# Kernel tuning notes

Measured on AMD Instinct MI355X. Metric: run time of the kernel, lower is better.

The kernel has to match this reference:

```python
import jax, jax.numpy as jnp
import numpy as np

B, S, D, H = 4, 1024, 1024, 16
DK = D // H
NEG = -1e9


def setup_inputs() -> dict:
    key = jax.random.key(0)
    ks = jax.random.split(key, 14)
    sc = 1.0 / np.sqrt(D)
    inp = {
        "query": jax.random.normal(ks[0], (B, S, D), jnp.float32),
        "key": jax.random.normal(ks[1], (B, S, D), jnp.float32),
        "value": jax.random.normal(ks[2], (B, S, D), jnp.float32),
        "mask": jax.random.randint(ks[3], (B, S, S), 0, 2, jnp.int32),
        "group_prob": jax.random.uniform(ks[4], (B, S, S), jnp.float32),
        "Wq": jax.random.normal(ks[5], (D, D), jnp.float32) * sc,
        "bq": jnp.zeros((D,), jnp.float32),
        "Wk": jax.random.normal(ks[6], (D, D), jnp.float32) * sc,
        "bk": jnp.zeros((D,), jnp.float32),
        "Wv": jax.random.normal(ks[7], (D, D), jnp.float32) * sc,
        "bv": jnp.zeros((D,), jnp.float32),
        "Wo": jax.random.normal(ks[8], (D, D), jnp.float32) * sc,
        "bo": jnp.zeros((D,), jnp.float32),
    }
    return inp


def reference(query, key, value, mask, group_prob, Wq, bq, Wk, bk, Wv, bv, Wo, bo):
    # QKV projections, split heads: [B,S,D] -> [B,H,S,DK]
    def proj(x, W, b):
        return (x @ W.T + b).reshape(B, S, H, DK).transpose(0, 2, 1, 3)

    q = proj(query, Wq, bq)
    k = proj(key, Wk, bk)
    v = proj(value, Wv, bv)

    scores = jnp.einsum("bhqd,bhkd->bhqk", q, k) / jnp.sqrt(jnp.float32(DK))

    # group_prob branch: allowed where mask OR diagonal is nonzero
    diag = jnp.eye(S, dtype=jnp.int32)
    allowed = (mask[:, None, :, :] | diag[None, None, :, :]) != 0  # [B,1,S,S]
    scores = jnp.where(allowed, scores, NEG)

    p_attn = jax.nn.softmax(scores, axis=-1)
    p_attn = p_attn * group_prob[:, None, :, :]  # post-softmax group reweighting

    x = jnp.einsum("bhqk,bhkd->bhqd", p_attn, v)
    x = x.transpose(0, 2, 1, 3).reshape(B, S, D)
    return x @ Wo.T + bo
```

## Files before the change

kernel.cpp:

```cpp
#include <hip/hip_runtime.h>
#include <hip/hip_bf16.h>


#define AS1q __attribute__((address_space(1)))
#define AS3q __attribute__((address_space(3)))

typedef __attribute__((ext_vector_type(8))) __bf16 bf16x8;
typedef __attribute__((ext_vector_type(4))) float f32x4;
typedef __attribute__((ext_vector_type(8))) unsigned short u16x8;

#define GSTR 40

__device__ __forceinline__ void gload_lds16(const void* g, void* l) {
  __builtin_amdgcn_global_load_lds((const AS1q void*)g, (AS3q void*)l, 16, 0, 0);
}
__device__ __forceinline__ bf16x8 lds_read8(const unsigned short* p) {
  bf16x8 r;
  __builtin_memcpy(&r, __builtin_assume_aligned(p, 16), 16);
  return r;
}
__device__ __forceinline__ void lds_write8(unsigned short* p, const void* v) {
  __builtin_memcpy(__builtin_assume_aligned(p, 16), v, 16);
}
__device__ __forceinline__ u16x8 cvt8h(const float4 a, const float4 b) {
  const float fv[8] = {a.x, a.y, a.z, a.w, b.x, b.y, b.z, b.w};
  union { u16x8 v; __bf16 e[8]; } hh;
#pragma unroll
  for (int i = 0; i < 8; ++i) hh.e[i] = (__bf16)fv[i];
  return hh.v;
}
__device__ __forceinline__ void cvt8hl(const float4 a, const float4 b, u16x8* hi, u16x8* lo) {
  const float fv[8] = {a.x, a.y, a.z, a.w, b.x, b.y, b.z, b.w};
  union { u16x8 v; __bf16 e[8]; } hh, ll;
#pragma unroll
  for (int i = 0; i < 8; ++i) {
    const __bf16 h = (__bf16)fv[i];
    hh.e[i] = h;
    ll.e[i] = (__bf16)(fv[i] - (float)h);
  }
  *hi = hh.v; *lo = ll.v;
}
__device__ __forceinline__ unsigned short bfbits(float f) {
  const __bf16 h = (__bf16)f;
  unsigned short u; __builtin_memcpy(&u, &h, 2); return u;
}

__global__ __launch_bounds__(256) void k_gemm_qkv(
    const float* __restrict__ X0, const float* __restrict__ X1, const float* __restrict__ X2,
    const float* __restrict__ W0, const float* __restrict__ W1, const float* __restrict__ W2,
    const float* __restrict__ B0, const float* __restrict__ B1, const float* __restrict__ B2,
    unsigned short* __restrict__ O0, unsigned short* __restrict__ O1,
    unsigned short* __restrict__ O2)
{
  const int z = blockIdx.z;
  const float* X = (z == 0) ? X0 : (z == 1) ? X1 : X2;
  const float* W = (z == 0) ? W0 : (z == 1) ? W1 : W2;
  const float* Bi = (z == 0) ? B0 : (z == 1) ? B1 : B2;
  unsigned short* O = (z == 0) ? O0 : (z == 1) ? O1 : O2;

  const int bid = blockIdx.x;
  const int swz = (bid & 7) * 64 + (bid >> 3);
  const int n0 = (swz & 15) * 64, m0 = (swz >> 4) * 128;

  __shared__ alignas(16) unsigned short Ah[128 * GSTR];
  __shared__ alignas(16) unsigned short Bh[64 * GSTR];
  const int tid = threadIdx.x, l = tid & 63, w = tid >> 6;
  const int wr = w >> 1, wc = w & 1;

  f32x4 acc[4][2];
#pragma unroll
  for (int i = 0; i < 4; ++i)
#pragma unroll
    for (int j = 0; j < 2; ++j) acc[i][j] = (f32x4){0.f, 0.f, 0.f, 0.f};

  const int arow = tid >> 1, ac0 = (tid & 1) * 16;
  const int brow = tid >> 2, bc0 = (tid & 3) * 8;
  const float* xsrc = X + (size_t)(m0 + arow) * 1024 + ac0;
  const float* wsrc = W + (size_t)(n0 + brow) * 1024 + bc0;

  float4 fx[4], fw[2];
#pragma unroll
  for (int i = 0; i < 4; ++i) fx[i] = *(const float4*)(xsrc + i * 4);
#pragma unroll
  for (int i = 0; i < 2; ++i) fw[i] = *(const float4*)(wsrc + i * 4);

  for (int kt = 0; kt < 32; ++kt) {
    u16x8 xh[2], wh1;
    xh[0] = cvt8h(fx[0], fx[1]);
    xh[1] = cvt8h(fx[2], fx[3]);
    wh1 = cvt8h(fw[0], fw[1]);
    if (kt < 31) {
      const float* nx = xsrc + (kt + 1) * 32;
      const float* nw = wsrc + (kt + 1) * 32;
#pragma unroll
      for (int i = 0; i < 4; ++i) fx[i] = *(const float4*)(nx + i * 4);
#pragma unroll
      for (int i = 0; i < 2; ++i) fw[i] = *(const float4*)(nw + i * 4);
    }
    __syncthreads();
    lds_write8(&Ah[arow * GSTR + ac0], &xh[0]);
    lds_write8(&Ah[arow * GSTR + ac0 + 8], &xh[1]);
    lds_write8(&Bh[brow * GSTR + bc0], &wh1);
    __syncthreads();

    bf16x8 ah[4], bh[2];
#pragma unroll
    for (int mf = 0; mf < 4; ++mf) {
      const int r = wr * 64 + mf * 16 + (l & 15);
      ah[mf] = lds_read8(&Ah[r * GSTR + (l >> 4) * 8]);
    }
#pragma unroll
    for (int nf = 0; nf < 2; ++nf) {
      const int r = wc * 32 + nf * 16 + (l & 15);
      bh[nf] = lds_read8(&Bh[r * GSTR + (l >> 4) * 8]);
    }
#pragma unroll
    for (int mf = 0; mf < 4; ++mf)
#pragma unroll
      for (int nf = 0; nf < 2; ++nf)
        acc[mf][nf] = __builtin_amdgcn_mfma_f32_16x16x32_bf16(ah[mf], bh[nf], acc[mf][nf], 0, 0, 0);
  }

#pragma unroll
  for (int nf = 0; nf < 2; ++nf) {
    const int col = n0 + wc * 32 + nf * 16 + (l & 15);
    const float bias = Bi[col];
#pragma unroll
    for (int mf = 0; mf < 4; ++mf) {
      const int rbase = m0 + wr * 64 + mf * 16 + (l >> 4) * 4;
#pragma unroll
      for (int j = 0; j < 4; ++j)
        O[(size_t)(rbase + j) * 1024 + col] = bfbits(acc[mf][nf][j] + bias);
    }
  }
}

__global__ __launch_bounds__(256) void k_gemm_out(
    const unsigned short* __restrict__ X, const float* __restrict__ W,
    const float* __restrict__ Bi, float* __restrict__ Out)
{
  const int bid = blockIdx.x;
  const int swz = (bid & 7) * 128 + (bid >> 3);
  const int n0 = (swz & 15) * 64, m0 = (swz >> 4) * 64;

  __shared__ alignas(16) unsigned short Ah[64 * GSTR];
  __shared__ alignas(16) unsigned short Bh[64 * GSTR], Bl[64 * GSTR];
  const int tid = threadIdx.x, l = tid & 63, w = tid >> 6;
  const int wr = w >> 1, wc = w & 1;

  f32x4 acc[2][2];
#pragma unroll
  for (int i = 0; i < 2; ++i)
#pragma unroll
    for (int j = 0; j < 2; ++j) acc[i][j] = (f32x4){0.f, 0.f, 0.f, 0.f};

  const int srow = tid >> 2, sc0 = (tid & 3) * 8;
  const unsigned short* xsrc = X + (size_t)(m0 + srow) * 1024 + sc0;
  const float* wsrc = W + (size_t)(n0 + srow) * 1024 + sc0;

  u16x8 xcur = *(const u16x8*)xsrc;
  float4 fw[2];
#pragma unroll
  for (int i = 0; i < 2; ++i) fw[i] = *(const float4*)(wsrc + i * 4);

  for (int kt = 0; kt < 32; ++kt) {
    const u16x8 xstage = xcur;
    u16x8 wh1, wl1;
    cvt8hl(fw[0], fw[1], &wh1, &wl1);
    if (kt < 31) {
      xcur = *(const u16x8*)(xsrc + (kt + 1) * 32);
      const float* nw = wsrc + (kt + 1) * 32;
#pragma unroll
      for (int i = 0; i < 2; ++i) fw[i] = *(const float4*)(nw + i * 4);
    }
    __syncthreads();
    lds_write8(&Ah[srow * GSTR + sc0], &xstage);
    lds_write8(&Bh[srow * GSTR + sc0], &wh1);
    lds_write8(&Bl[srow * GSTR + sc0], &wl1);
    __syncthreads();

    bf16x8 ah[2], bh[2], bl[2];
#pragma unroll
    for (int mf = 0; mf < 2; ++mf) {
      const int r = wr * 32 + mf * 16 + (l & 15);
      ah[mf] = lds_read8(&Ah[r * GSTR + (l >> 4) * 8]);
    }
#pragma unroll
    for (int nf = 0; nf < 2; ++nf) {
      const int r = wc * 32 + nf * 16 + (l & 15);
      bh[nf] = lds_read8(&Bh[r * GSTR + (l >> 4) * 8]);
      bl[nf] = lds_read8(&Bl[r * GSTR + (l >> 4) * 8]);
    }
#pragma unroll
    for (int mf = 0; mf < 2; ++mf)
#pragma unroll
      for (int nf = 0; nf < 2; ++nf) {
        acc[mf][nf] = __builtin_amdgcn_mfma_f32_16x16x32_bf16(ah[mf], bh[nf], acc[mf][nf], 0, 0, 0);
        acc[mf][nf] = __builtin_amdgcn_mfma_f32_16x16x32_bf16(ah[mf], bl[nf], acc[mf][nf], 0, 0, 0);
      }
  }

#pragma unroll
  for (int nf = 0; nf < 2; ++nf) {
    const int col = n0 + wc * 32 + nf * 16 + (l & 15);
    const float bias = Bi[col];
#pragma unroll
    for (int mf = 0; mf < 2; ++mf) {
      const int rbase = m0 + wr * 32 + mf * 16 + (l >> 4) * 4;
#pragma unroll
      for (int j = 0; j < 4; ++j)
        Out[(size_t)(rbase + j) * 1024 + col] = acc[mf][nf][j] + bias;
    }
  }
}

__global__ __launch_bounds__(256) void k_attn(
    const unsigned short* Qh, const unsigned short* __restrict__ Kb,
    const unsigned short* __restrict__ Vb,
    const int* __restrict__ Mask, const float* __restrict__ Gp,
    unsigned short* Xo)
{
  const int i = blockIdx.x;
  const int xc = i & 7, kk_ = i >> 3;
  const int h = kk_ & 15, g = kk_ >> 4;
  const int qb = g * 8 + xc;
  const int qt = qb >> 2, b = qb & 3;

  __shared__ alignas(16) unsigned short Kh[2][64 * 64];
  __shared__ alignas(16) unsigned short Vh[64 * 64];
  __shared__ alignas(16) unsigned short Ph[64 * 64];
  __shared__ alignas(16) int Ms[64 * 64];
  __shared__ alignas(16) float Gs[64 * 64];
  const int tid = threadIdx.x, l = tid & 63, w = tid >> 6;

  const unsigned short* kb_ = Kb + (size_t)b * 1048576 + h * 64;
  const unsigned short* vb_ = Vb + (size_t)b * 1048576 + h * 64;
  const int qrowbase = b * 1024 + qt * 64;

  bf16x8 aq[2];
  {
    const int qrow = qt * 64 + w * 16 + (l & 15);
    const unsigned short* qp_ = Qh + ((size_t)(b * 1024 + qrow)) * 1024 + h * 64;
    aq[0] = lds_read8(qp_ + (l >> 4) * 8);
    aq[1] = lds_read8(qp_ + 32 + (l >> 4) * 8);
  }

  f32x4 accO[4];
#pragma unroll
  for (int nf = 0; nf < 4; ++nf) accO[nf] = (f32x4){0.f, 0.f, 0.f, 0.f};
  float zacc[4] = {0.f, 0.f, 0.f, 0.f};

  const int qloc0 = w * 16 + (l >> 4) * 4;
  const int qg0 = qt * 64 + qloc0;
  const int mcol = l & 15;

  const int srcg8 = ((l & 7) ^ (l >> 3)) * 8;
  const int rowl = l >> 3;

  const int* msrc = Mask + ((size_t)(qrowbase + w * 16 + (l >> 4)) << 10) + (l & 15) * 4;
  const float* gsrc = Gp + ((size_t)(qrowbase + w * 16 + (l >> 4)) << 10) + (l & 15) * 4;

  const int kb4 = (tid & 15) * 4, db4 = (tid >> 4) * 4;
  union U4 { unsigned int u[2]; unsigned short s[4]; };
  U4 vr[4];

#pragma unroll
  for (int I = 0; I < 2; ++I)
    gload_lds16(kb_ + (size_t)(I * 32 + w * 8 + rowl) * 1024 + srcg8,
                &Kh[0][I * 2048 + w * 512]);
#pragma unroll
  for (int ii = 0; ii < 4; ++ii)
    __builtin_memcpy(&vr[ii], vb_ + (size_t)(kb4 + ii) * 1024 + db4, 8);

  int buf = 0;
  for (int kt = 0; kt < 16; ++kt) {
    __syncthreads();

#pragma unroll
    for (int I = 0; I < 4; ++I) {
      gload_lds16(msrc + (size_t)kt * 64 + I * 4096, (char*)Ms + w * 4096 + I * 1024);
      gload_lds16(gsrc + (size_t)kt * 64 + I * 4096, (char*)Gs + w * 4096 + I * 1024);
    }
#pragma unroll
    for (int ii = 0; ii < 4; ++ii) {
      const int d = db4 + ii;
      union { unsigned short s[4]; unsigned long long v; } pk;
#pragma unroll
      for (int u = 0; u < 4; ++u) pk.s[u] = vr[u].s[ii];
      const int c = kb4 ^ ((d & 7) << 3);
      __builtin_memcpy(__builtin_assume_aligned(&Vh[d * 64 + c], 8), &pk.v, 8);
    }
    __syncthreads();

    if (kt < 15) {
#pragma unroll
      for (int I = 0; I < 2; ++I)
        gload_lds16(kb_ + (size_t)((kt + 1) * 64 + I * 32 + w * 8 + rowl) * 1024 + srcg8,
                    &Kh[buf ^ 1][I * 2048 + w * 512]);
#pragma unroll
      for (int ii = 0; ii < 4; ++ii)
        __builtin_memcpy(&vr[ii], vb_ + (size_t)((kt + 1) * 64 + kb4 + ii) * 1024 + db4, 8);
    }

#pragma unroll
    for (int nf = 0; nf < 4; ++nf) {
      f32x4 sacc = (f32x4){0.f, 0.f, 0.f, 0.f};
      const int kr = nf * 16 + (l & 15);
#pragma unroll
      for (int ks = 0; ks < 2; ++ks) {
        const int c = (ks * 32 + (l >> 4) * 8) ^ ((kr & 7) << 3);
        sacc = __builtin_amdgcn_mfma_f32_16x16x32_bf16(aq[ks], lds_read8(&Kh[buf][kr * 64 + c]), sacc, 0, 0, 0);
      }
      const int kg = kt * 64 + nf * 16 + mcol;
#pragma unroll
      for (int j = 0; j < 4; ++j) {
        const int qg = qg0 + j;
        const int qloc = qloc0 + j;
        const int mk = Ms[qloc * 64 + nf * 16 + mcol];
        const float gvv = Gs[qloc * 64 + nf * 16 + mcol];
        const int allowed = mk | (qg == kg);
        const float e = allowed ? exp2f(fmaf(sacc[j], 0.18033688f, -17.31234049f)) : 0.f;
        zacc[j] += e;
        Ph[qloc * 64 + ((nf * 16 + mcol) ^ ((qloc & 7) << 3))] = bfbits(e * gvv);
      }
    }
    bf16x8 pah[2];
    {
      const int ar = w * 16 + (l & 15);
#pragma unroll
      for (int ks = 0; ks < 2; ++ks) {
        const int c = (ks * 32 + (l >> 4) * 8) ^ ((ar & 7) << 3);
        pah[ks] = lds_read8(&Ph[ar * 64 + c]);
      }
    }
#pragma unroll
    for (int nf = 0; nf < 4; ++nf) {
      const int dr = nf * 16 + (l & 15);
#pragma unroll
      for (int ks = 0; ks < 2; ++ks) {
        const int c = (ks * 32 + (l >> 4) * 8) ^ ((dr & 7) << 3);
        accO[nf] = __builtin_amdgcn_mfma_f32_16x16x32_bf16(pah[ks], lds_read8(&Vh[dr * 64 + c]), accO[nf], 0, 0, 0);
      }
    }
    buf ^= 1;
  }

#pragma unroll
  for (int j = 0; j < 4; ++j) {
#pragma unroll
    for (int off = 1; off < 16; off <<= 1) zacc[j] += __shfl_xor(zacc[j], off, 64);
  }
  float rz[4];
#pragma unroll
  for (int j = 0; j < 4; ++j) rz[j] = 1.f / zacc[j];

#pragma unroll
  for (int nf = 0; nf < 4; ++nf) {
    const int d = nf * 16 + (l & 15);
#pragma unroll
    for (int j = 0; j < 4; ++j) {
      const int qg = qg0 + j;
      Xo[((size_t)(b * 1024 + qg)) * 1024 + h * 64 + d] = bfbits(accO[nf][j] * rz[j]);
    }
  }
}

extern "C" void kernel_launch(void* const* d_in, const int* in_sizes, int n_in,
                              void* d_out, int out_size, void* d_ws, size_t ws_size,
                              hipStream_t stream) {
  const float* query = (const float*)d_in[0];
  const float* key_in = (const float*)d_in[1];
  const float* value = (const float*)d_in[2];
  const int* mask = (const int*)d_in[3];
  const float* gp = (const float*)d_in[4];
  const float* Wq = (const float*)d_in[5];
  const float* bq = (const float*)d_in[6];
  const float* Wk = (const float*)d_in[7];
  const float* bk = (const float*)d_in[8];
  const float* Wv = (const float*)d_in[9];
  const float* bv = (const float*)d_in[10];
  const float* Wo = (const float*)d_in[11];
  const float* bo = (const float*)d_in[12];
  float* out = (float*)d_out;

  unsigned short* kp = (unsigned short*)d_ws;
  unsigned short* vp = kp + 4194304;
  unsigned short* qp = vp + 4194304;
  unsigned short* xo = qp;

  hipLaunchKernelGGL(k_gemm_qkv, dim3(512, 1, 3), dim3(256), 0, stream,
                     query, key_in, value, Wq, Wk, Wv, bq, bk, bv, qp, kp, vp);
  hipLaunchKernelGGL(k_attn, dim3(1024), dim3(256), 0, stream,
                     qp, kp, vp, mask, gp, xo);
  hipLaunchKernelGGL(k_gemm_out, dim3(1024), dim3(256), 0, stream,
                     xo, Wo, bo, out);
}
```

Baseline: 186.5 us.

## Precombine mask, diagonal and group_prob into one array in a prep kernel

A new prep kernel merges the int mask, the diagonal rule and group_prob into a single float array, using -1 as a sentinel for disallowed positions. The attention kernel then reads this one array straight into registers, prefetched one tile ahead, instead of staging both mask and group_prob through LDS. This halves the per-head mask/probability traffic and frees LDS. In exchange it adds an extra launch that reads and writes the full B×S×S data, and it assumes group_prob is never negative.

```diff
diff --git a/kernel.cpp b/kernel.cpp
--- a/kernel.cpp
+++ b/kernel.cpp
@@ -43,6 +43,22 @@
 __device__ __forceinline__ unsigned short bfbits(float f) {
   const __bf16 h = (__bf16)f;
   unsigned short u; __builtin_memcpy(&u, &h, 2); return u;
+}
+
+__global__ __launch_bounds__(256) void k_prep(
+    const int* __restrict__ Mask, const float* __restrict__ Gp, float* __restrict__ G2)
+{
+  const size_t f = (size_t)blockIdx.x * 256 + threadIdx.x;
+  const size_t e = f << 2;
+  const int k0 = (int)(e & 1023), q = (int)((e >> 10) & 1023);
+  const int4 m4 = *(const int4*)(Mask + e);
+  const float4 g4 = *(const float4*)(Gp + e);
+  float4 r;
+  r.x = (m4.x | (q == k0 + 0)) ? g4.x : -1.f;
+  r.y = (m4.y | (q == k0 + 1)) ? g4.y : -1.f;
+  r.z = (m4.z | (q == k0 + 2)) ? g4.z : -1.f;
+  r.w = (m4.w | (q == k0 + 3)) ? g4.w : -1.f;
+  *(float4*)(G2 + e) = r;
 }
 
 __global__ __launch_bounds__(256) void k_gemm_qkv(
@@ -217,8 +233,7 @@
 __global__ __launch_bounds__(256) void k_attn(
     const unsigned short* Qh, const unsigned short* __restrict__ Kb,
     const unsigned short* __restrict__ Vb,
-    const int* __restrict__ Mask, const float* __restrict__ Gp,
-    unsigned short* Xo)
+    const float* __restrict__ G2, unsigned short* Xo)
 {
   const int i = blockIdx.x;
   const int xc = i & 7, kk_ = i >> 3;
@@ -229,13 +244,10 @@
   __shared__ alignas(16) unsigned short Kh[2][64 * 64];
   __shared__ alignas(16) unsigned short Vh[64 * 64];
   __shared__ alignas(16) unsigned short Ph[64 * 64];
-  __shared__ alignas(16) int Ms[64 * 64];
-  __shared__ alignas(16) float Gs[64 * 64];
   const int tid = threadIdx.x, l = tid & 63, w = tid >> 6;
 
   const unsigned short* kb_ = Kb + (size_t)b * 1048576 + h * 64;
   const unsigned short* vb_ = Vb + (size_t)b * 1048576 + h * 64;
-  const int qrowbase = b * 1024 + qt * 64;
 
   bf16x8 aq[2];
   {
@@ -254,12 +266,13 @@
   const int qg0 = qt * 64 + qloc0;
   const int mcol = l & 15;
 
+  const float* grow[4];
+#pragma unroll
+  for (int j = 0; j < 4; ++j)
+    grow[j] = G2 + (((size_t)(b * 1024 + qg0 + j)) << 10) + mcol;
+
   const int srcg8 = ((l & 7) ^ (l >> 3)) * 8;
   const int rowl = l >> 3;
-
-  const int* msrc = Mask + ((size_t)(qrowbase + w * 16 + (l >> 4)) << 10) + (l & 15) * 4;
-  const float* gsrc = Gp + ((size_t)(qrowbase + w * 16 + (l >> 4)) << 10) + (l & 15) * 4;
-
   const int kb4 = (tid & 15) * 4, db4 = (tid >> 4) * 4;
   union U4 { unsigned int u[2]; unsigned short s[4]; };
   U4 vr[4];
@@ -272,15 +285,16 @@
   for (int ii = 0; ii < 4; ++ii)
     __builtin_memcpy(&vr[ii], vb_ + (size_t)(kb4 + ii) * 1024 + db4, 8);
 
+  float gcur[4][4], gnext[4][4];
+#pragma unroll
+  for (int nf = 0; nf < 4; ++nf)
+#pragma unroll
+    for (int j = 0; j < 4; ++j) gcur[nf][j] = grow[j][nf * 16];
+
   int buf = 0;
   for (int kt = 0; kt < 16; ++kt) {
     __syncthreads();
 
-#pragma unroll
-    for (int I = 0; I < 4; ++I) {
-      gload_lds16(msrc + (size_t)kt * 64 + I * 4096, (char*)Ms + w * 4096 + I * 1024);
-      gload_lds16(gsrc + (size_t)kt * 64 + I * 4096, (char*)Gs + w * 4096 + I * 1024);
-    }
 #pragma unroll
     for (int ii = 0; ii < 4; ++ii) {
       const int d = db4 + ii;
@@ -300,6 +314,10 @@
 #pragma unroll
       for (int ii = 0; ii < 4; ++ii)
         __builtin_memcpy(&vr[ii], vb_ + (size_t)((kt + 1) * 64 + kb4 + ii) * 1024 + db4, 8);
+#pragma unroll
+      for (int nf = 0; nf < 4; ++nf)
+#pragma unroll
+        for (int j = 0; j < 4; ++j) gnext[nf][j] = grow[j][(kt + 1) * 64 + nf * 16];
     }
 
 #pragma unroll
@@ -311,17 +329,13 @@
         const int c = (ks * 32 + (l >> 4) * 8) ^ ((kr & 7) << 3);
         sacc = __builtin_amdgcn_mfma_f32_16x16x32_bf16(aq[ks], lds_read8(&Kh[buf][kr * 64 + c]), sacc, 0, 0, 0);
       }
-      const int kg = kt * 64 + nf * 16 + mcol;
 #pragma unroll
       for (int j = 0; j < 4; ++j) {
-        const int qg = qg0 + j;
+        const float g2 = gcur[nf][j];
+        const float e = (g2 >= 0.f) ? exp2f(fmaf(sacc[j], 0.18033688f, -17.31234049f)) : 0.f;
+        zacc[j] += e;
         const int qloc = qloc0 + j;
-        const int mk = Ms[qloc * 64 + nf * 16 + mcol];
-        const float gvv = Gs[qloc * 64 + nf * 16 + mcol];
-        const int allowed = mk | (qg == kg);
-        const float e = allowed ? exp2f(fmaf(sacc[j], 0.18033688f, -17.31234049f)) : 0.f;
-        zacc[j] += e;
-        Ph[qloc * 64 + ((nf * 16 + mcol) ^ ((qloc & 7) << 3))] = bfbits(e * gvv);
+        Ph[qloc * 64 + ((nf * 16 + mcol) ^ ((qloc & 7) << 3))] = bfbits(e * g2);
       }
     }
     bf16x8 pah[2];
@@ -343,6 +357,10 @@
       }
     }
     buf ^= 1;
+#pragma unroll
+    for (int nf = 0; nf < 4; ++nf)
+#pragma unroll
+      for (int j = 0; j < 4; ++j) gcur[nf][j] = gnext[nf][j];
   }
 
 #pragma unroll
@@ -387,11 +405,13 @@
   unsigned short* vp = kp + 4194304;
   unsigned short* qp = vp + 4194304;
   unsigned short* xo = qp;
-
+  float* g2 = (float*)(qp + 4194304);
+
+  hipLaunchKernelGGL(k_prep, dim3(4096), dim3(256), 0, stream, mask, gp, g2);
   hipLaunchKernelGGL(k_gemm_qkv, dim3(512, 1, 3), dim3(256), 0, stream,
                      query, key_in, value, Wq, Wk, Wv, bq, bk, bv, qp, kp, vp);
   hipLaunchKernelGGL(k_attn, dim3(1024), dim3(256), 0, stream,
-                     qp, kp, vp, mask, gp, xo);
+                     qp, kp, vp, g2, xo);
   hipLaunchKernelGGL(k_gemm_out, dim3(1024), dim3(256), 0, stream,
                      xo, Wo, bo, out);
 }
```

Result: no change. 186.3 us (-0.1%).
